# Kernel optimization log

Hardware: AMD Instinct MI355X
Metric: run time of the kernel (lower is better)

Reference implementation:

```python
import jax, jax.numpy as jnp
import numpy as np
from jax import lax

N_NODES = 4096
WINDOW = 288
SLIDE = 12
ENC_STEPS = 12
DEC_STEPS = 12
HID = 64
EMB = 64
PRED = 12
C1, C2 = 32, 64
KSZ, STR = 10, 2
OUT_LEN = 66  # ((288-10)//2+1 -> 140; (140-10)//2+1 -> 66)
EPS = 1e-5


def _conv1d(x, w, b, stride):
    # x: [N, Cin, L], w: [Cout, Cin, K]
    y = lax.conv_general_dilated(x, w, (stride,), 'VALID',
                                 dimension_numbers=('NCH', 'OIH', 'NCH'))
    return y + b[None, :, None]


def _bn(x, g, b):
    # BatchNorm1d training-mode stats over (batch, length) per channel
    m = x.mean(axis=(0, 2), keepdims=True)
    v = x.var(axis=(0, 2), keepdims=True)
    return (x - m) * jax.lax.rsqrt(v + EPS) * g[None, :, None] + b[None, :, None]


def _embed(x, conv1_w, conv1_b, conv2_w, conv2_b, bn1_g, bn1_b, bn2_g, bn2_b,
           fcconv_w, fcconv_b, fc_w, fc_b):
    # x: [N, WINDOW] -> [N, EMB]
    x = x[:, None, :]                                   # [N,1,W]
    x = _bn(jax.nn.relu(_conv1d(x, conv1_w, conv1_b, STR)), bn1_g, bn1_b)
    x = _bn(jax.nn.relu(_conv1d(x, conv2_w, conv2_b, STR)), bn2_g, bn2_b)
    x = jax.nn.relu(_conv1d(x, fcconv_w, fcconv_b, 1))  # [N,1,OUT_LEN]
    x = jnp.einsum('ncl,le->nce', x, fc_w) + fc_b       # [N,1,EMB]
    # NOTE: original code calls F.relu(x) but discards the result -> no relu here
    return x[:, 0, :]


def _gconv(x, adj, W, b):
    # diffusion conv: [x, A x, 2A(Ax) - x] (K=2, includes identity term)
    x1 = adj @ x
    x2 = 2.0 * (adj @ x1) - x
    return jnp.concatenate([x, x1, x2], axis=-1) @ W + b


def _dcgru_cell(x, h, adj, Wg, bg, Wc, bc):
    ru = jax.nn.sigmoid(_gconv(jnp.concatenate([x, h], -1), adj, Wg, bg))
    r, u = jnp.split(ru, 2, axis=-1)
    c = jnp.tanh(_gconv(jnp.concatenate([x, r * h], -1), adj, Wc, bc))
    return u * h + (1.0 - u) * c


def setup_inputs() -> dict:
    key = jax.random.key(0)
    ks = jax.random.split(key, 20)
    n_mat = 3  # K+1 diffusion matrices
    gin = (EMB + HID) * n_mat
    inp = {
        'inputs': jax.random.normal(ks[0], (N_NODES, (ENC_STEPS + DEC_STEPS - 1) * SLIDE + WINDOW), jnp.float32),
        'targets': jax.random.normal(ks[1], (N_NODES, DEC_STEPS * PRED), jnp.float32),
        'conv1_w': jax.random.normal(ks[3], (C1, 1, KSZ), jnp.float32) * 0.1,
        'conv1_b': jnp.zeros((C1,), jnp.float32),
        'conv2_w': jax.random.normal(ks[4], (C2, C1, KSZ), jnp.float32) * 0.1,
        'conv2_b': jnp.zeros((C2,), jnp.float32),
        'bn1_g': jnp.ones((C1,), jnp.float32), 'bn1_b': jnp.zeros((C1,), jnp.float32),
        'bn2_g': jnp.ones((C2,), jnp.float32), 'bn2_b': jnp.zeros((C2,), jnp.float32),
        'fcconv_w': jax.random.normal(ks[5], (1, C2, 1), jnp.float32) * 0.1,
        'fcconv_b': jnp.zeros((1,), jnp.float32),
        'fc_w': jax.random.normal(ks[6], (OUT_LEN, EMB), jnp.float32) * (1.0 / np.sqrt(OUT_LEN)),
        'fc_b': jnp.zeros((EMB,), jnp.float32),
        'enc_Wg': jax.random.normal(ks[7], (gin, 2 * HID), jnp.float32) * (1.0 / np.sqrt(gin)),
        'enc_bg': jnp.ones((2 * HID,), jnp.float32),
        'enc_Wc': jax.random.normal(ks[8], (gin, HID), jnp.float32) * (1.0 / np.sqrt(gin)),
        'enc_bc': jnp.zeros((HID,), jnp.float32),
        'dec_Wg': jax.random.normal(ks[9], (gin, 2 * HID), jnp.float32) * (1.0 / np.sqrt(gin)),
        'dec_bg': jnp.ones((2 * HID,), jnp.float32),
        'dec_Wc': jax.random.normal(ks[10], (gin, HID), jnp.float32) * (1.0 / np.sqrt(gin)),
        'dec_bc': jnp.zeros((HID,), jnp.float32),
        'pred_w': jax.random.normal(ks[11], (HID, PRED), jnp.float32) * (1.0 / np.sqrt(HID)),
        'pred_b': jnp.full((PRED,), 0.1, jnp.float32),
    }
    a = jax.random.uniform(ks[2], (N_NODES, N_NODES), jnp.float32)
    inp['adj'] = a / a.sum(axis=-1, keepdims=True)  # row-stochastic adjacency
    return inp


def reference(inputs, targets, adj,
              conv1_w, conv1_b, conv2_w, conv2_b, bn1_g, bn1_b, bn2_g, bn2_b,
              fcconv_w, fcconv_b, fc_w, fc_b,
              enc_Wg, enc_bg, enc_Wc, enc_bc,
              dec_Wg, dec_bg, dec_Wc, dec_bc,
              pred_w, pred_b):
    n = inputs.shape[0]
    # windowed views: idx[i] = i*SLIDE, 24 windows of length WINDOW
    idx = SLIDE * jnp.arange(ENC_STEPS + DEC_STEPS)
    wins = inputs[:, idx[:, None] + jnp.arange(WINDOW)]        # [N, 24, W]
    wins = jnp.transpose(wins, (1, 0, 2))                      # [24, N, W]
    embs = jax.vmap(lambda w: _embed(w, conv1_w, conv1_b, conv2_w, conv2_b,
                                     bn1_g, bn1_b, bn2_g, bn2_b,
                                     fcconv_w, fcconv_b, fc_w, fc_b))(wins)  # [24,N,EMB]
    enc_x, dec_x = embs[:ENC_STEPS], embs[ENC_STEPS:]

    h0 = jnp.zeros((n, HID), inputs.dtype)
    def enc_step(h, x):
        return _dcgru_cell(x, h, adj, enc_Wg, enc_bg, enc_Wc, enc_bc), None
    h_enc, _ = lax.scan(enc_step, h0, enc_x)

    # decoder: each step uses the SAME encoder hidden state (as in original code)
    dec_h = jax.vmap(lambda x: _dcgru_cell(x, h_enc, adj, dec_Wg, dec_bg, dec_Wc, dec_bc))(dec_x)  # [12,N,HID]
    preds = dec_h @ pred_w + pred_b                             # [12,N,PRED]
    return jnp.transpose(preds, (1, 0, 2)).reshape(n, DEC_STEPS * PRED)
```

## Files before the change

kernel.cpp:

```cpp
#include <hip/hip_runtime.h>
#include <hip/hip_bf16.h>
#include <math.h>

#define NN     4096
#define INLEN  564
#define NT     24
#define NC1    32
#define NC2    64
#define KS     10
#define EPS    1e-5f

typedef short s8v __attribute__((ext_vector_type(8)));
typedef short s4v __attribute__((ext_vector_type(4)));
typedef float f4v __attribute__((ext_vector_type(4)));

static const long O_COLS   = 0;
static const long O_COLSQ  = 8960;
static const long O_STATS  = 17920;
static const long O_H      = 20992;
static const long ZERO_FLOATS = 283136;
static const long O_A1     = 283136;
static const long O_D1     = 283904;
static const long O_CB2    = 284672;
static const long O_W2B    = 286208;
static const long O_G1P    = 532480;
static const long O_Y2     = 18882560;
static const long O_EMBS   = 27795456;
static const long O_ADJB   = 532480;
static const long O_PP     = 8921088;
static const long O_X      = 13115392;
static const long O_XT     = 13639680;
static const long O_T1     = 13901824;
static const long O_T1T    = 14426112;
static const long O_T2     = 14688256;
static const long O_RH     = 15212544;
static const long O_RHT    = 15474688;
static const long O_P1S    = 15605760;
static const long O_P1ST   = 15867904;
static const long O_P2S    = 15998976;
static const long O_UE     = 16261120;
static const long O_EB     = 16392192;
static const long O_EBT    = 20062208;
static const long O_AE1    = 21897216;
static const long O_AE1T   = 25567232;
static const long O_AE2    = 27795456;
static const long O_RHB    = 31465472;
static const long O_P1B    = 34611200;
static const long O_P2B    = O_X;
static const long O_HD     = O_PP;

struct Src { const float* p; int ld; int off; int tmul; };

static __device__ __forceinline__ float cvt_bf(short s) {
  return __uint_as_float(((unsigned)(unsigned short)s) << 16);
}
static __device__ __forceinline__ short bf16bits(float v) {
  __hip_bfloat16_raw r = __hip_bfloat16_raw(__float2bfloat16(v));
  return (short)r.x;
}

__global__ __launch_bounds__(256) void k_conv1n(const float* __restrict__ inp,
    const float* __restrict__ w1, const float* __restrict__ b1,
    __hip_bfloat16* __restrict__ g1p) {
  __shared__ float xin[INLEN];
  __shared__ float wl[320];
  __shared__ float bl[32];
  int n = blockIdx.x, tid = threadIdx.x;
  for (int i=tid; i<INLEN; i+=256) xin[i] = inp[(long)n*INLEN + i];
  for (int i=tid; i<320; i+=256) wl[i] = w1[i];
  if (tid < 32)  bl[tid] = b1[tid];
  __syncthreads();
  int c = tid & 31, pb = tid >> 5;
  float wreg[KS];
  #pragma unroll
  for (int k=0;k<KS;k++) wreg[k] = wl[c*KS+k];
  float bias = bl[c];
  for (int p = pb; p < 280; p += 8) {
    float acc = 0.f;
    if (p < 278) {
      acc = bias;
      #pragma unroll
      for (int k=0;k<KS;k++) acc = fmaf(wreg[k], xin[2*p+k], acc);
      acc = fmaxf(acc, 0.f);
    }
    g1p[((long)n*280 + p)*32 + c] = __float2bfloat16(acc);
  }
}

__global__ __launch_bounds__(256) void k_colsum2(const __hip_bfloat16* __restrict__ g1p,
    float* __restrict__ colS, float* __restrict__ colSQ) {
  int gid = blockIdx.x*256 + threadIdx.x;
  int cg = gid % 1120, chunk = gid / 1120;
  int col0 = cg*8;
  float s[8], sq[8];
  #pragma unroll
  for (int j=0;j<8;j++) { s[j]=0.f; sq[j]=0.f; }
  int n0 = chunk*128;
  const short* gp = (const short*)g1p;
  for (int n=n0; n<n0+128; n++) {
    s8v v = *(const s8v*)(gp + (long)n*8960 + col0);
    #pragma unroll
    for (int j=0;j<8;j++) { float f = cvt_bf(v[j]); s[j]+=f; sq[j]+=f*f; }
  }
  #pragma unroll
  for (int j=0;j<8;j++) { atomicAdd(&colS[col0+j], s[j]); atomicAdd(&colSQ[col0+j], sq[j]); }
}

__global__ __launch_bounds__(64) void k_bn1aff(const float* __restrict__ colS,
    const float* __restrict__ colSQ, const float* __restrict__ g, const float* __restrict__ b,
    float* __restrict__ a1, float* __restrict__ d1) {
  int i = blockIdx.x*64 + threadIdx.x;
  if (i >= NT*NC1) return;
  int t = i / NC1, c = i % NC1;
  float s=0.f, sq=0.f;
  for (int p=6*t; p<6*t+140; p++) { s += colS[p*32+c]; sq += colSQ[p*32+c]; }
  float cnt = 4096.f*140.f;
  float m = s/cnt;
  float v = sq/cnt - m*m;
  float a = g[c]*rsqrtf(v+EPS);
  a1[i] = a;
  d1[i] = b[c] - m*a;
}

__global__ __launch_bounds__(256) void k_w2b(const float* __restrict__ w2,
    const float* __restrict__ b2, const float* __restrict__ a1, const float* __restrict__ d1,
    __hip_bfloat16* __restrict__ w2b, float* __restrict__ cb2) {
  int i = blockIdx.x*256 + threadIdx.x;
  if (i >= NT*NC2) return;
  int t = i>>6, c2 = i&63;
  float cb = b2[c2];
  for (int c1=0;c1<NC1;c1++) {
    float a = a1[t*32+c1], d = d1[t*32+c1];
    float wsum = 0.f;
    for (int k=0;k<KS;k++) {
      float wv = w2[(c2*32+c1)*KS+k];
      wsum += wv;
      w2b[(((long)t*10 + k)*64 + c2)*32 + c1] = __float2bfloat16(wv*a);
    }
    cb += wsum*d;
  }
  cb2[i] = cb;
}

__global__ __launch_bounds__(256) void k_conv2m(const __hip_bfloat16* __restrict__ g1p,
    const __hip_bfloat16* __restrict__ w2b, const float* __restrict__ cb2,
    __hip_bfloat16* __restrict__ y2, float* __restrict__ stats, int t) {
  __shared__ __attribute__((aligned(16))) short patch[4*140*40];
  __shared__ float sS[64], sQ[64];
  int tid = threadIdx.x, w = tid>>6, lane = tid&63;
  int n0 = blockIdx.x*4;
  if (tid < 64) { sS[tid]=0.f; sQ[tid]=0.f; }
  const short* gp = (const short*)g1p;
  for (int f = tid; f < 2240; f += 256) {
    int nn = f / 560, rr = f % 560;
    int row = rr >> 2, kq = rr & 3;
    s8v v = *(const s8v*)(gp + ((long)(n0+nn)*280 + 6*t + row)*32 + kq*8);
    *(s8v*)&patch[(nn*140 + row)*40 + kq*8] = v;
  }
  __syncthreads();
  int q = lane>>4, m = lane&15;
  f4v acc[5][4];
  #pragma unroll
  for (int a=0;a<5;a++)
    #pragma unroll
    for (int b=0;b<4;b++) acc[a][b] = (f4v){0.f,0.f,0.f,0.f};
  const short* wb = (const short*)w2b + (long)t*10*64*32;
  for (int s=0; s<10; s++) {
    int j = s>>1, r = s&1;
    s8v bfr[4];
    #pragma unroll
    for (int ng=0; ng<4; ng++)
      bfr[ng] = *(const s8v*)(wb + (long)(s*64 + ng*16 + m)*32 + q*8);
    #pragma unroll
    for (int mg=0; mg<5; mg++) {
      int l2 = mg*16 + m;
      int u = l2 + j; u = (u>69)?69:u;
      s8v afr = *(const s8v*)&patch[(w*140 + 2*u + r)*40 + q*8];
      #pragma unroll
      for (int ng=0; ng<4; ng++)
        acc[mg][ng] = __builtin_amdgcn_mfma_f32_16x16x32_bf16(afr, bfr[ng], acc[mg][ng], 0,0,0);
    }
  }
  int node = n0 + w;
  float s1a[4]={0,0,0,0}, s2a[4]={0,0,0,0};
  #pragma unroll
  for (int mg=0; mg<5; mg++) {
    int l2b = mg*16 + q*4;
    #pragma unroll
    for (int ng=0; ng<4; ng++) {
      int c2 = ng*16 + m;
      float cbv = cb2[t*64 + c2];
      float vv[4];
      #pragma unroll
      for (int rr=0; rr<4; rr++) {
        float v = fmaxf(acc[mg][ng][rr] + cbv, 0.f);
        vv[rr] = v;
        if (l2b + rr < 66) { s1a[ng] += v; s2a[ng] += v*v; }
      }
      long base = ((long)node*64 + c2)*68 + l2b;
      if (mg < 4) {
        s4v o;
        #pragma unroll
        for (int rr=0; rr<4; rr++) o[rr] = bf16bits(vv[rr]);
        *(s4v*)((short*)y2 + base) = o;
      } else {
        for (int rr=0; rr<4; rr++) if (l2b+rr < 66) y2[base+rr] = __float2bfloat16(vv[rr]);
      }
    }
  }
  #pragma unroll
  for (int ng=0; ng<4; ng++) {
    atomicAdd(&sS[ng*16+m], s1a[ng]);
    atomicAdd(&sQ[ng*16+m], s2a[ng]);
  }
  __syncthreads();
  if (tid < 64) {
    atomicAdd(&stats[t*128+tid], sS[tid]);
    atomicAdd(&stats[t*128+64+tid], sQ[tid]);
  }
}

__global__ __launch_bounds__(256) void k_pass2(const __hip_bfloat16* __restrict__ y2,
    const float* __restrict__ stats, const float* __restrict__ bn2g, const float* __restrict__ bn2b,
    const float* __restrict__ fcvw, const float* __restrict__ fcvb,
    const float* __restrict__ fcW, const float* __restrict__ fcB,
    float* __restrict__ embs, int t) {
  __shared__ __attribute__((aligned(16))) short yb[4*64*68];
  __shared__ float fw[66*64];
  __shared__ float fwa[64], cfcs[64];
  __shared__ float zbuf[4][68];
  int tid = threadIdx.x;
  int n0 = blockIdx.x*4;
  const short* yg = (const short*)y2;
  for (int f=tid; f<2176; f+=256)
    *(s8v*)&yb[f*8] = *(const s8v*)(yg + (long)n0*64*68 + f*8);
  for (int i=tid; i<66*64; i+=256) fw[i] = fcW[i];
  if (tid < 64) {
    float cnt = 4096.f*66.f;
    float m = stats[t*128+tid]/cnt;
    float v = stats[t*128+64+tid]/cnt - m*m;
    float a = bn2g[tid]*rsqrtf(v+EPS);
    float d = bn2b[tid] - m*a;
    fwa[tid]  = fcvw[tid]*a;
    cfcs[tid] = fcvw[tid]*d;
  }
  __syncthreads();
  float cfc = fcvb[0];
  #pragma unroll 8
  for (int c=0;c<64;c++) cfc += cfcs[c];
  for (int idx=tid; idx<4*66; idx+=256) {
    int nn = idx/66, l = idx%66;
    float z = cfc;
    #pragma unroll 8
    for (int c=0;c<64;c++) z = fmaf(fwa[c], cvt_bf(yb[(nn*64+c)*68 + l]), z);
    zbuf[nn][l] = fmaxf(z, 0.f);
  }
  __syncthreads();
  int nn = tid>>6, e = tid&63;
  float acc = fcB[e];
  for (int l=0;l<66;l++) acc = fmaf(zbuf[nn][l], fw[l*64+e], acc);
  embs[((long)t*NN + n0+nn)*64 + e] = acc;
}

__global__ __launch_bounds__(256) void k_cvtadj(const float* __restrict__ adj,
    __hip_bfloat16* __restrict__ adjb) {
  long gid = ((long)blockIdx.x*256 + threadIdx.x)*4;
  float4 v = *(const float4*)(adj + gid);
  adjb[gid+0] = __float2bfloat16(v.x);
  adjb[gid+1] = __float2bfloat16(v.y);
  adjb[gid+2] = __float2bfloat16(v.z);
  adjb[gid+3] = __float2bfloat16(v.w);
}

template<int BN>
__global__ __launch_bounds__(256) void k_mmb(const __hip_bfloat16* __restrict__ A,
    const __hip_bfloat16* __restrict__ Bt, float* __restrict__ P,
    int N, int kchunk, long zoff) {
  constexpr int BM = 64;
  constexpr int WN = BN/2;
  constexpr int MI = 2;
  constexpr int NJ = WN/16;
  constexpr int AIT = BM*8/256;
  constexpr int BIT = BN*8/256;
  __shared__ __attribute__((aligned(16))) short As[BM*64];
  __shared__ __attribute__((aligned(16))) short Bs[BN*64];
  int tid = threadIdx.x;
  int w = tid >> 6, lane = tid & 63;
  int wm = w >> 1, wn = w & 1;
  int q = lane >> 4, m = lane & 15;
  long Mb = (long)blockIdx.x * BM;
  int Nb = blockIdx.y * BN;
  int k0 = blockIdx.z * kchunk;
  const short* Ag = (const short*)A;
  const short* Bg = (const short*)Bt;
  s8v ar[AIT], br[BIT];
  #pragma unroll
  for (int it=0; it<AIT; ++it) {
    int f = tid + it*256; int kq = f & 7, row = f >> 3;
    ar[it] = *(const s8v*)(Ag + (Mb + row)*4096 + k0 + kq*8);
  }
  #pragma unroll
  for (int it=0; it<BIT; ++it) {
    int f = tid + it*256; int kq = f & 7, col = f >> 3;
    br[it] = *(const s8v*)(Bg + (long)(Nb + col)*4096 + k0 + kq*8);
  }
  f4v acc[MI][NJ];
  #pragma unroll
  for (int i=0;i<MI;i++)
    #pragma unroll
    for (int j=0;j<NJ;j++) acc[i][j] = (f4v){0.f,0.f,0.f,0.f};
  for (int kc = k0; kc < k0 + kchunk; kc += 64) {
    __syncthreads();
    #pragma unroll
    for (int it=0; it<AIT; ++it) {
      int f = tid + it*256; int kq = f & 7, row = f >> 3;
      *(s8v*)&As[(row*8 + (kq ^ (row&7)))*8] = ar[it];
    }
    #pragma unroll
    for (int it=0; it<BIT; ++it) {
      int f = tid + it*256; int kq = f & 7, col = f >> 3;
      *(s8v*)&Bs[(col*8 + (kq ^ (col&7)))*8] = br[it];
    }
    __syncthreads();
    if (kc + 64 < k0 + kchunk) {
      #pragma unroll
      for (int it=0; it<AIT; ++it) {
        int f = tid + it*256; int kq = f & 7, row = f >> 3;
        ar[it] = *(const s8v*)(Ag + (Mb + row)*4096 + (kc+64) + kq*8);
      }
      #pragma unroll
      for (int it=0; it<BIT; ++it) {
        int f = tid + it*256; int kq = f & 7, col = f >> 3;
        br[it] = *(const s8v*)(Bg + (long)(Nb + col)*4096 + (kc+64) + kq*8);
      }
    }
    #pragma unroll
    for (int h=0; h<2; ++h) {
      s8v af[MI], bfv[NJ];
      #pragma unroll
      for (int i=0;i<MI;i++) {
        int row = wm*32 + i*16 + m;
        af[i] = *(const s8v*)&As[(row*8 + ((h*4+q) ^ (row&7)))*8];
      }
      #pragma unroll
      for (int j=0;j<NJ;j++) {
        int col = wn*WN + j*16 + m;
        bfv[j] = *(const s8v*)&Bs[(col*8 + ((h*4+q) ^ (col&7)))*8];
      }
      #pragma unroll
      for (int i=0;i<MI;i++)
        #pragma unroll
        for (int j=0;j<NJ;j++)
          acc[i][j] = __builtin_amdgcn_mfma_f32_16x16x32_bf16(af[i], bfv[j], acc[i][j], 0, 0, 0);
    }
  }
  float* pp = P + (long)blockIdx.z * zoff;
  #pragma unroll
  for (int i=0;i<MI;i++) {
    long row0 = Mb + wm*32 + i*16 + q*4;
    #pragma unroll
    for (int j=0;j<NJ;j++) {
      int col = Nb + wn*WN + j*16 + m;
      #pragma unroll
      for (int r=0;r<4;r++)
        pp[(row0 + r)*N + col] = acc[i][j][r];
    }
  }
}

__global__ __launch_bounds__(256) void k_redT(const float* __restrict__ P,
    float* __restrict__ dst, const float* __restrict__ ref,
    __hip_bfloat16* __restrict__ dstT, int ldc, int ksplit, long zoff, int mode,
    int writeF, int writeT) {
  __shared__ float tile[64][65];
  int tid = threadIdx.x;
  int n0 = blockIdx.x*64, c0 = blockIdx.y*64;
  for (int i=0; i<16; i++) {
    int flat = i*256 + tid;
    int cc = flat & 63, nn = flat >> 6;
    long idx = (long)(n0+nn)*ldc + c0+cc;
    float v = P[idx];
    for (int s=1; s<ksplit; s++) v += P[(long)s*zoff + idx];
    if (mode) v = 2.f*v - ref[idx];
    if (writeF) dst[idx] = v;
    tile[nn][cc] = v;
  }
  __syncthreads();
  if (writeT) {
    for (int i=0; i<16; i++) {
      int flat = i*256 + tid;
      int nn = flat & 63, cc = flat >> 6;
      dstT[(long)(c0+cc)*4096 + n0+nn] = __float2bfloat16(tile[nn][cc]);
    }
  }
}

__global__ __launch_bounds__(256) void k_buildXT(const float* __restrict__ et,
    const float* __restrict__ h, float* __restrict__ X, __hip_bfloat16* __restrict__ Xt) {
  __shared__ float tile[64][65];
  int tid = threadIdx.x;
  int n0 = blockIdx.x*64, c0 = blockIdx.y*64;
  for (int i=0; i<16; i++) {
    int flat = i*256 + tid;
    int cc = flat & 63, nn = flat >> 6;
    int col = c0 + cc, n = n0 + nn;
    float v = (col < 64) ? et[(long)n*64 + col] : h[(long)n*64 + (col-64)];
    X[(long)n*128 + col] = v;
    tile[nn][cc] = v;
  }
  __syncthreads();
  for (int i=0; i<16; i++) {
    int flat = i*256 + tid;
    int nn = flat & 63, cc = flat >> 6;
    Xt[(long)(c0+cc)*4096 + n0+nn] = __float2bfloat16(tile[nn][cc]);
  }
}

__global__ __launch_bounds__(256) void k_gatherE(const float* __restrict__ embs,
    const float* __restrict__ h, float* __restrict__ Eb, __hip_bfloat16* __restrict__ Ebt) {
  __shared__ float tile[64][65];
  int tid = threadIdx.x;
  int n0 = blockIdx.x*64, c0 = blockIdx.y*64;
  for (int i=0; i<16; i++) {
    int flat = i*256 + tid;
    int cc = flat & 63, nn = flat >> 6;
    int col = c0 + cc, n = n0 + nn;
    float v;
    if (col < 768)      v = embs[((long)(12 + (col>>6))*NN + n)*64 + (col & 63)];
    else if (col < 832) v = h[(long)n*64 + (col - 768)];
    else                v = 0.f;
    Eb[(long)n*896 + col] = v;
    tile[nn][cc] = v;
  }
  __syncthreads();
  for (int i=0; i<16; i++) {
    int flat = i*256 + tid;
    int nn = flat & 63, cc = flat >> 6;
    Ebt[(long)(c0+cc)*4096 + n0+nn] = __float2bfloat16(tile[nn][cc]);
  }
}

__global__ __launch_bounds__(256) void k_ggemm(
    Src s0, Src s1, Src s2, Src s3, Src s4, Src s5,
    const float* __restrict__ W, const float* __restrict__ bias, int N, int mode,
    float* __restrict__ o1, int ld1, int t1, __hip_bfloat16* __restrict__ o1t,
    __hip_bfloat16* __restrict__ o2, const float* __restrict__ h) {
  __shared__ float Ags[32][68];
  __shared__ float Bgs[32][64];
  int tid = threadIdx.x;
  int Mb = blockIdx.x*64, Nb = blockIdx.y*64;
  int tr = tid >> 4, tc = tid & 15;
  float acc[4][4];
  #pragma unroll
  for (int a=0;a<4;a++)
    #pragma unroll
    for (int b=0;b<4;b++) acc[a][b] = 0.f;
  for (int c0=0; c0<384; c0+=32) {
    Src S;
    switch (c0 >> 6) {
      case 0: S = s0; break; case 1: S = s1; break; case 2: S = s2; break;
      case 3: S = s3; break; case 4: S = s4; break; default: S = s5; break;
    }
    int cc0 = c0 & 63;
    __syncthreads();
    #pragma unroll
    for (int h0=0; h0<8; h0++) {
      int idx = tid + h0*256;
      int kk = idx & 31, mm = idx >> 5;
      int row = Mb + mm, tt = row >> 12, n = row & 4095;
      Ags[kk][mm] = S.p[(long)n*S.ld + S.off + S.tmul*(tt*64) + cc0 + kk];
    }
    #pragma unroll
    for (int h0=0; h0<8; h0++) {
      int idx = tid + h0*256;
      int kk = idx >> 6, cc = idx & 63;
      Bgs[kk][cc] = W[(long)(c0+kk)*N + Nb + cc];
    }
    __syncthreads();
    #pragma unroll
    for (int kk=0; kk<32; kk++) {
      f4v a4 = *(const f4v*)&Ags[kk][tr*4];
      f4v b4 = *(const f4v*)&Bgs[kk][tc*4];
      #pragma unroll
      for (int rr=0; rr<4; rr++)
        #pragma unroll
        for (int j=0; j<4; j++)
          acc[rr][j] = fmaf(a4[rr], b4[j], acc[rr][j]);
    }
  }
  #pragma unroll
  for (int rr=0; rr<4; rr++) {
    int row = Mb + tr*4 + rr, tt = row >> 12, n = row & 4095;
    #pragma unroll
    for (int j=0; j<4; j++) {
      int col = Nb + tc*4 + j;
      float g = acc[rr][j] + bias[col];
      if (mode == 0) {
        float sg = 1.f/(1.f + expf(-g));
        if (col < 64) {
          float v = sg * h[(long)n*64 + col];
          o1[(long)n*ld1 + (long)t1*tt*64 + col] = v;
          o1t[((long)t1*tt*64 + col)*4096 + n] = __float2bfloat16(v);
        } else {
          o2[(long)row*64 + (col - 64)] = __float2bfloat16(sg);
        }
      } else {
        float uu = __bfloat162float(o2[(long)row*64 + col]);
        o1[(long)row*64 + col] = uu*h[(long)n*64 + col] + (1.f - uu)*tanhf(g);
      }
    }
  }
}

__global__ __launch_bounds__(256) void k_pred(const float* __restrict__ hd,
    const float* __restrict__ pw, const float* __restrict__ pb, float* __restrict__ out) {
  int gid = blockIdx.x*256 + threadIdx.x;
  int wid = gid >> 6;
  int lane = threadIdx.x & 63;
  if (wid >= 12*NN) return;
  int t = wid >> 12, n = wid & 4095;
  float hv = hd[(long)wid*64 + lane];
  float res = 0.f;
  #pragma unroll
  for (int p=0;p<12;p++) {
    float v = hv * pw[lane*12 + p];
    #pragma unroll
    for (int off=32; off>0; off>>=1) v += __shfl_xor(v, off, 64);
    if (lane == p) res = v + pb[p];
  }
  if (lane < 12) out[(long)n*144 + t*12 + lane] = res;
}

extern "C" void kernel_launch(void* const* d_in, const int* in_sizes, int n_in,
                              void* d_out, int out_size, void* d_ws, size_t ws_size,
                              hipStream_t stream) {
  const float* inp  = (const float*)d_in[0];
  const float* c1w  = (const float*)d_in[2];
  const float* c1b  = (const float*)d_in[3];
  const float* c2w  = (const float*)d_in[4];
  const float* c2b  = (const float*)d_in[5];
  const float* bn1g = (const float*)d_in[6];
  const float* bn1b = (const float*)d_in[7];
  const float* bn2g = (const float*)d_in[8];
  const float* bn2b = (const float*)d_in[9];
  const float* fcvw = (const float*)d_in[10];
  const float* fcvb = (const float*)d_in[11];
  const float* fcW  = (const float*)d_in[12];
  const float* fcB  = (const float*)d_in[13];
  const float* eWg  = (const float*)d_in[14];
  const float* ebg  = (const float*)d_in[15];
  const float* eWc  = (const float*)d_in[16];
  const float* ebc  = (const float*)d_in[17];
  const float* dWg  = (const float*)d_in[18];
  const float* dbg  = (const float*)d_in[19];
  const float* dWc  = (const float*)d_in[20];
  const float* dbc  = (const float*)d_in[21];
  const float* pw   = (const float*)d_in[22];
  const float* pb   = (const float*)d_in[23];
  const float* adj  = (const float*)d_in[n_in-1];
  for (int i=0;i<n_in;i++) if (in_sizes[i] == NN*NN) adj = (const float*)d_in[i];

  float* ws = (float*)d_ws;
  float* colS  = ws + O_COLS;
  float* colSQ = ws + O_COLSQ;
  float* stats = ws + O_STATS;
  float* h     = ws + O_H;
  float* a1    = ws + O_A1;
  float* d1    = ws + O_D1;
  float* cb2   = ws + O_CB2;
  __hip_bfloat16* w2b = (__hip_bfloat16*)(ws + O_W2B);
  __hip_bfloat16* g1p = (__hip_bfloat16*)(ws + O_G1P);
  __hip_bfloat16* y2  = (__hip_bfloat16*)(ws + O_Y2);
  float* embs  = ws + O_EMBS;
  __hip_bfloat16* adjb = (__hip_bfloat16*)(ws + O_ADJB);
  float* Pp    = ws + O_PP;
  float* X     = ws + O_X;
  __hip_bfloat16* Xt  = (__hip_bfloat16*)(ws + O_XT);
  float* T1    = ws + O_T1;
  __hip_bfloat16* T1t = (__hip_bfloat16*)(ws + O_T1T);
  float* T2    = ws + O_T2;
  float* rh    = ws + O_RH;
  __hip_bfloat16* rht = (__hip_bfloat16*)(ws + O_RHT);
  float* P1s   = ws + O_P1S;
  __hip_bfloat16* P1st = (__hip_bfloat16*)(ws + O_P1ST);
  float* P2s   = ws + O_P2S;
  __hip_bfloat16* ue  = (__hip_bfloat16*)(ws + O_UE);
  float* Eb    = ws + O_EB;
  __hip_bfloat16* Ebt = (__hip_bfloat16*)(ws + O_EBT);
  float* AE1   = ws + O_AE1;
  __hip_bfloat16* AE1t = (__hip_bfloat16*)(ws + O_AE1T);
  float* AE2   = ws + O_AE2;
  float* RHb   = ws + O_RHB;
  float* P1B   = ws + O_P1B;
  float* P2B   = ws + O_P2B;
  float* hd    = ws + O_HD;
  __hip_bfloat16* RHbt = Ebt;
  __hip_bfloat16* P1Bt = Ebt;
  __hip_bfloat16* ud   = AE1t;

  auto S = [](const float* p, int ld, int off, int tmul){ Src s; s.p=p; s.ld=ld; s.off=off; s.tmul=tmul; return s; };

  hipMemsetAsync(ws, 0, ZERO_FLOATS*sizeof(float), stream);

  k_conv1n<<<4096, 256, 0, stream>>>(inp, c1w, c1b, g1p);
  k_colsum2<<<140, 256, 0, stream>>>(g1p, colS, colSQ);
  k_bn1aff<<<12, 64, 0, stream>>>(colS, colSQ, bn1g, bn1b, a1, d1);
  k_w2b   <<<6, 256, 0, stream>>>(c2w, c2b, a1, d1, w2b, cb2);
  for (int t=0; t<NT; t++) {
    k_conv2m<<<1024, 256, 0, stream>>>(g1p, w2b, cb2, y2, stats, t);
    k_pass2 <<<1024, 256, 0, stream>>>(y2, stats, bn2g, bn2b, fcvw, fcvb, fcW, fcB, embs, t);
  }

  k_cvtadj<<<16384, 256, 0, stream>>>(adj, adjb);

  for (int t=0; t<12; t++) {
    const float* et = embs + (long)t*NN*64;
    k_buildXT<<<dim3(64,2), 256, 0, stream>>>(et, h, X, Xt);
    k_mmb<128><<<dim3(64,1,8), 256, 0, stream>>>(adjb, Xt, Pp, 128, 512, 4096L*128);
    k_redT<<<dim3(64,2), 256, 0, stream>>>(Pp, T1, (const float*)nullptr, T1t, 128, 8, 4096L*128, 0, 1, 1);
    k_mmb<128><<<dim3(64,1,8), 256, 0, stream>>>(adjb, T1t, Pp, 128, 512, 4096L*128);
    k_redT<<<dim3(64,2), 256, 0, stream>>>(Pp, T2, X, (__hip_bfloat16*)nullptr, 128, 8, 4096L*128, 1, 1, 0);
    k_ggemm<<<dim3(64,2), 256, 0, stream>>>(
        S(X,128,0,0), S(X,128,64,0), S(T1,128,0,0), S(T1,128,64,0), S(T2,128,0,0), S(T2,128,64,0),
        eWg, ebg, 128, 0, rh, 64, 0, rht, ue, h);
    k_mmb<64><<<dim3(64,1,8), 256, 0, stream>>>(adjb, rht, Pp, 64, 512, 4096L*64);
    k_redT<<<dim3(64,1), 256, 0, stream>>>(Pp, P1s, (const float*)nullptr, P1st, 64, 8, 4096L*64, 0, 1, 1);
    k_mmb<64><<<dim3(64,1,8), 256, 0, stream>>>(adjb, P1st, Pp, 64, 512, 4096L*64);
    k_redT<<<dim3(64,1), 256, 0, stream>>>(Pp, P2s, rh, (__hip_bfloat16*)nullptr, 64, 8, 4096L*64, 1, 1, 0);
    k_ggemm<<<dim3(64,1), 256, 0, stream>>>(
        S(et,64,0,0), S(rh,64,0,0), S(T1,128,0,0), S(P1s,64,0,0), S(T2,128,0,0), S(P2s,64,0,0),
        eWc, ebc, 64, 1, h, 0, 0, (__hip_bfloat16*)nullptr, ue, h);
  }

  const long ZOFF896 = 4096L*896;
  const long ZOFF_P1 = O_PP - O_P1B;
  const long ZOFF_P2 = O_PP - O_X;
  k_gatherE<<<dim3(64,14), 256, 0, stream>>>(embs, h, Eb, Ebt);
  k_mmb<128><<<dim3(64,7,2), 256, 0, stream>>>(adjb, Ebt, Pp, 896, 2048, ZOFF896);
  k_redT<<<dim3(64,14), 256, 0, stream>>>(Pp, AE1, (const float*)nullptr, AE1t, 896, 2, ZOFF896, 0, 1, 1);
  k_mmb<128><<<dim3(64,7,2), 256, 0, stream>>>(adjb, AE1t, Pp, 896, 2048, ZOFF896);
  k_redT<<<dim3(64,14), 256, 0, stream>>>(Pp, AE2, Eb, (__hip_bfloat16*)nullptr, 896, 2, ZOFF896, 1, 1, 0);
  k_ggemm<<<dim3(768,2), 256, 0, stream>>>(
      S(Eb,896,0,1), S(Eb,896,768,0), S(AE1,896,0,1), S(AE1,896,768,0), S(AE2,896,0,1), S(AE2,896,768,0),
      dWg, dbg, 128, 0, RHb, 768, 1, RHbt, ud, h);
  k_mmb<128><<<dim3(64,6,2), 256, 0, stream>>>(adjb, RHbt, P1B, 768, 2048, ZOFF_P1);
  k_redT<<<dim3(64,12), 256, 0, stream>>>(P1B, P1B, (const float*)nullptr, P1Bt, 768, 2, ZOFF_P1, 0, 1, 1);
  k_mmb<128><<<dim3(64,6,2), 256, 0, stream>>>(adjb, P1Bt, P2B, 768, 2048, ZOFF_P2);
  k_redT<<<dim3(64,12), 256, 0, stream>>>(P2B, P2B, RHb, (__hip_bfloat16*)nullptr, 768, 2, ZOFF_P2, 1, 1, 0);
  k_ggemm<<<dim3(768,1), 256, 0, stream>>>(
      S(Eb,896,0,1), S(RHb,768,0,1), S(AE1,896,0,1), S(P1B,768,0,1), S(AE2,896,0,1), S(P2B,768,0,1),
      dWc, dbc, 64, 1, hd, 0, 0, (__hip_bfloat16*)nullptr, ud, h);

  k_pred<<<12288, 256, 0, stream>>>(hd, pw, pb, (float*)d_out);
}
```

Measured before the change: 5.324 ms.

## Fuse split-K reduction into GEMM via atomic counters, retile gate GEMMs

```diff
diff --git a/kernel.cpp b/kernel.cpp
--- a/kernel.cpp
+++ b/kernel.cpp
@@ -13,19 +13,21 @@
 typedef short s8v __attribute__((ext_vector_type(8)));
 typedef short s4v __attribute__((ext_vector_type(4)));
 typedef float f4v __attribute__((ext_vector_type(4)));
+typedef float f2v __attribute__((ext_vector_type(2)));
 
 static const long O_COLS   = 0;
 static const long O_COLSQ  = 8960;
 static const long O_STATS  = 17920;
 static const long O_H      = 20992;
-static const long ZERO_FLOATS = 283136;
-static const long O_A1     = 283136;
-static const long O_D1     = 283904;
-static const long O_CB2    = 284672;
-static const long O_W2B    = 286208;
-static const long O_G1P    = 532480;
-static const long O_Y2     = 18882560;
-static const long O_EMBS   = 27795456;
+static const long O_CNT    = 283136;
+static const long ZERO_FLOATS = 291328;
+static const long O_A1     = 291328;
+static const long O_D1     = 292096;
+static const long O_CB2    = 292864;
+static const long O_W2B    = 532480;
+static const long O_G1P    = 778240;
+static const long O_Y2     = 19128320;
+static const long O_EMBS   = 28041216;
 static const long O_ADJB   = 532480;
 static const long O_PP     = 8921088;
 static const long O_X      = 13115392;
@@ -46,6 +48,7 @@
 static const long O_AE2    = 27795456;
 static const long O_RHB    = 31465472;
 static const long O_P1B    = 34611200;
+static const long O_P1BT   = O_PP;
 static const long O_P2B    = O_X;
 static const long O_HD     = O_PP;
 
@@ -274,13 +277,15 @@
 
 template<int BN>
 __global__ __launch_bounds__(256) void k_mmb(const __hip_bfloat16* __restrict__ A,
-    const __hip_bfloat16* __restrict__ Bt, float* __restrict__ P,
-    int N, int kchunk, long zoff) {
+    const __hip_bfloat16* __restrict__ Bt, float* P,
+    int N, int kchunk, long zoff,
+    float* dst, const float* __restrict__ ref, __hip_bfloat16* __restrict__ dstT,
+    int mode, int writeT, unsigned* __restrict__ cnt, int zsplit) {
   constexpr int BM = 64;
   constexpr int WN = BN/2;
   constexpr int MI = 2;
   constexpr int NJ = WN/16;
-  constexpr int AIT = BM*8/256;
+  constexpr int AIT = 2;
   constexpr int BIT = BN*8/256;
   __shared__ __attribute__((aligned(16))) short As[BM*64];
   __shared__ __attribute__((aligned(16))) short Bs[BN*64];
@@ -293,104 +298,135 @@
   int k0 = blockIdx.z * kchunk;
   const short* Ag = (const short*)A;
   const short* Bg = (const short*)Bt;
-  s8v ar[AIT], br[BIT];
-  #pragma unroll
-  for (int it=0; it<AIT; ++it) {
-    int f = tid + it*256; int kq = f & 7, row = f >> 3;
-    ar[it] = *(const s8v*)(Ag + (Mb + row)*4096 + k0 + kq*8);
-  }
-  #pragma unroll
-  for (int it=0; it<BIT; ++it) {
-    int f = tid + it*256; int kq = f & 7, col = f >> 3;
-    br[it] = *(const s8v*)(Bg + (long)(Nb + col)*4096 + k0 + kq*8);
-  }
+  s8v arA[AIT], brA[BIT], arB[AIT], brB[BIT];
+
+  auto loadAr = [&](s8v* d, int kb){
+    #pragma unroll
+    for (int i2=0;i2<AIT;i2++){ int f=tid+i2*256; int kq=f&7, row=f>>3;
+      d[i2] = *(const s8v*)(Ag + (Mb+row)*4096 + kb + kq*8); } };
+  auto loadBr = [&](s8v* d, int kb){
+    #pragma unroll
+    for (int i2=0;i2<BIT;i2++){ int f=tid+i2*256; int kq=f&7, col=f>>3;
+      d[i2] = *(const s8v*)(Bg + (long)(Nb+col)*4096 + kb + kq*8); } };
+
   f4v acc[MI][NJ];
   #pragma unroll
   for (int i=0;i<MI;i++)
     #pragma unroll
     for (int j=0;j<NJ;j++) acc[i][j] = (f4v){0.f,0.f,0.f,0.f};
-  for (int kc = k0; kc < k0 + kchunk; kc += 64) {
-    __syncthreads();
-    #pragma unroll
-    for (int it=0; it<AIT; ++it) {
-      int f = tid + it*256; int kq = f & 7, row = f >> 3;
-      *(s8v*)&As[(row*8 + (kq ^ (row&7)))*8] = ar[it];
-    }
-    #pragma unroll
-    for (int it=0; it<BIT; ++it) {
-      int f = tid + it*256; int kq = f & 7, col = f >> 3;
-      *(s8v*)&Bs[(col*8 + (kq ^ (col&7)))*8] = br[it];
-    }
-    __syncthreads();
-    if (kc + 64 < k0 + kchunk) {
-      #pragma unroll
-      for (int it=0; it<AIT; ++it) {
-        int f = tid + it*256; int kq = f & 7, row = f >> 3;
-        ar[it] = *(const s8v*)(Ag + (Mb + row)*4096 + (kc+64) + kq*8);
-      }
-      #pragma unroll
-      for (int it=0; it<BIT; ++it) {
-        int f = tid + it*256; int kq = f & 7, col = f >> 3;
-        br[it] = *(const s8v*)(Bg + (long)(Nb + col)*4096 + (kc+64) + kq*8);
-      }
-    }
-    #pragma unroll
-    for (int h=0; h<2; ++h) {
+
+  auto writeS = [&](s8v* a, s8v* b){
+    #pragma unroll
+    for (int i2=0;i2<AIT;i2++){ int f=tid+i2*256; int kq=f&7, row=f>>3;
+      *(s8v*)&As[(row*8 + (kq ^ (row&7)))*8] = a[i2]; }
+    #pragma unroll
+    for (int i2=0;i2<BIT;i2++){ int f=tid+i2*256; int kq=f&7, col=f>>3;
+      *(s8v*)&Bs[(col*8 + (kq ^ (col&7)))*8] = b[i2]; } };
+  auto compute = [&](){
+    #pragma unroll
+    for (int h2=0; h2<2; ++h2) {
       s8v af[MI], bfv[NJ];
       #pragma unroll
       for (int i=0;i<MI;i++) {
         int row = wm*32 + i*16 + m;
-        af[i] = *(const s8v*)&As[(row*8 + ((h*4+q) ^ (row&7)))*8];
+        af[i] = *(const s8v*)&As[(row*8 + ((h2*4+q) ^ (row&7)))*8];
       }
       #pragma unroll
       for (int j=0;j<NJ;j++) {
         int col = wn*WN + j*16 + m;
-        bfv[j] = *(const s8v*)&Bs[(col*8 + ((h*4+q) ^ (col&7)))*8];
+        bfv[j] = *(const s8v*)&Bs[(col*8 + ((h2*4+q) ^ (col&7)))*8];
       }
       #pragma unroll
       for (int i=0;i<MI;i++)
         #pragma unroll
         for (int j=0;j<NJ;j++)
           acc[i][j] = __builtin_amdgcn_mfma_f32_16x16x32_bf16(af[i], bfv[j], acc[i][j], 0, 0, 0);
-    }
-  }
-  float* pp = P + (long)blockIdx.z * zoff;
-  #pragma unroll
-  for (int i=0;i<MI;i++) {
-    long row0 = Mb + wm*32 + i*16 + q*4;
-    #pragma unroll
-    for (int j=0;j<NJ;j++) {
-      int col = Nb + wn*WN + j*16 + m;
-      #pragma unroll
-      for (int r=0;r<4;r++)
-        pp[(row0 + r)*N + col] = acc[i][j][r];
-    }
-  }
-}
-
-__global__ __launch_bounds__(256) void k_redT(const float* __restrict__ P,
-    float* __restrict__ dst, const float* __restrict__ ref,
-    __hip_bfloat16* __restrict__ dstT, int ldc, int ksplit, long zoff, int mode,
-    int writeF, int writeT) {
-  __shared__ float tile[64][65];
-  int tid = threadIdx.x;
-  int n0 = blockIdx.x*64, c0 = blockIdx.y*64;
-  for (int i=0; i<16; i++) {
-    int flat = i*256 + tid;
-    int cc = flat & 63, nn = flat >> 6;
-    long idx = (long)(n0+nn)*ldc + c0+cc;
-    float v = P[idx];
-    for (int s=1; s<ksplit; s++) v += P[(long)s*zoff + idx];
-    if (mode) v = 2.f*v - ref[idx];
-    if (writeF) dst[idx] = v;
-    tile[nn][cc] = v;
-  }
-  __syncthreads();
-  if (writeT) {
-    for (int i=0; i<16; i++) {
-      int flat = i*256 + tid;
-      int nn = flat & 63, cc = flat >> 6;
-      dstT[(long)(c0+cc)*4096 + n0+nn] = __float2bfloat16(tile[nn][cc]);
+    } };
+
+  loadAr(arA, k0);      loadBr(brA, k0);
+  loadAr(arB, k0+64);   loadBr(brB, k0+64);
+  int kiters = kchunk >> 6;
+  for (int it = 0; it < kiters; it += 2) {
+    __syncthreads();
+    writeS(arA, brA);
+    __syncthreads();
+    { int kn = (it+2 < kiters) ? k0 + (it+2)*64 : k0;
+      loadAr(arA, kn); loadBr(brA, kn); }
+    compute();
+    __syncthreads();
+    writeS(arB, brB);
+    __syncthreads();
+    { int kn = (it+3 < kiters) ? k0 + (it+3)*64 : k0;
+      loadAr(arB, kn); loadBr(brB, kn); }
+    compute();
+  }
+
+  if (zsplit > 1) {
+    float* pp = P + (long)blockIdx.z * zoff;
+    #pragma unroll
+    for (int i=0;i<MI;i++) {
+      long row0 = Mb + wm*32 + i*16 + q*4;
+      #pragma unroll
+      for (int j=0;j<NJ;j++) {
+        int col = Nb + wn*WN + j*16 + m;
+        #pragma unroll
+        for (int r=0;r<4;r++) pp[(row0+r)*N + col] = acc[i][j][r];
+      }
+    }
+    __threadfence();
+    __syncthreads();
+    __shared__ unsigned lastv;
+    if (tid == 0) lastv = atomicAdd(&cnt[blockIdx.y*gridDim.x + blockIdx.x], 1u);
+    __syncthreads();
+    if (lastv != (unsigned)(zsplit-1)) return;
+    __threadfence();
+    #pragma unroll
+    for (int i=0;i<MI;i++) {
+      long row0 = Mb + wm*32 + i*16 + q*4;
+      #pragma unroll
+      for (int j=0;j<NJ;j++) {
+        int col = Nb + wn*WN + j*16 + m;
+        float vr[4];
+        #pragma unroll
+        for (int r=0;r<4;r++) {
+          long idx = (row0+r)*N + col;
+          float v = P[idx];
+          for (int s2=1;s2<zsplit;s2++) v += P[(long)s2*zoff + idx];
+          if (mode) v = 2.f*v - ref[idx];
+          dst[idx] = v;
+          vr[r] = v;
+        }
+        if (writeT) {
+          s4v o;
+          #pragma unroll
+          for (int r=0;r<4;r++) o[r] = bf16bits(vr[r]);
+          *(s4v*)((short*)dstT + (long)col*4096 + row0) = o;
+        }
+      }
+    }
+  } else {
+    #pragma unroll
+    for (int i=0;i<MI;i++) {
+      long row0 = Mb + wm*32 + i*16 + q*4;
+      #pragma unroll
+      for (int j=0;j<NJ;j++) {
+        int col = Nb + wn*WN + j*16 + m;
+        float vr[4];
+        #pragma unroll
+        for (int r=0;r<4;r++) {
+          long idx = (row0+r)*N + col;
+          float v = acc[i][j][r];
+          if (mode) v = 2.f*v - ref[idx];
+          dst[idx] = v;
+          vr[r] = v;
+        }
+        if (writeT) {
+          s4v o;
+          #pragma unroll
+          for (int r=0;r<4;r++) o[r] = bf16bits(vr[r]);
+          *(s4v*)((short*)dstT + (long)col*4096 + row0) = o;
+        }
+      }
     }
   }
 }
@@ -440,57 +476,87 @@
   }
 }
 
-__global__ __launch_bounds__(256) void k_ggemm(
+template<int RPT>
+__global__ __launch_bounds__(256) void k_ggemm2(
     Src s0, Src s1, Src s2, Src s3, Src s4, Src s5,
     const float* __restrict__ W, const float* __restrict__ bias, int N, int mode,
     float* __restrict__ o1, int ld1, int t1, __hip_bfloat16* __restrict__ o1t,
     __hip_bfloat16* __restrict__ o2, const float* __restrict__ h) {
-  __shared__ float Ags[32][68];
-  __shared__ float Bgs[32][64];
+  constexpr int BM = 16*RPT;
+  __shared__ float Ags[32][BM+4];
+  __shared__ float Bgs[32][68];
   int tid = threadIdx.x;
-  int Mb = blockIdx.x*64, Nb = blockIdx.y*64;
+  long Mb = (long)blockIdx.x * BM;
+  int Nb = blockIdx.y * 64;
   int tr = tid >> 4, tc = tid & 15;
-  float acc[4][4];
-  #pragma unroll
-  for (int a=0;a<4;a++)
+  float acc[RPT][4];
+  #pragma unroll
+  for (int a=0;a<RPT;a++)
     #pragma unroll
     for (int b=0;b<4;b++) acc[a][b] = 0.f;
-  for (int c0=0; c0<384; c0+=32) {
-    Src S;
-    switch (c0 >> 6) {
-      case 0: S = s0; break; case 1: S = s1; break; case 2: S = s2; break;
-      case 3: S = s3; break; case 4: S = s4; break; default: S = s5; break;
-    }
-    int cc0 = c0 & 63;
-    __syncthreads();
-    #pragma unroll
-    for (int h0=0; h0<8; h0++) {
+  float ar[2*RPT], br[8];
+  auto pick = [&](int c)->Src {
+    switch (c >> 1) {
+      case 0: return s0; case 1: return s1; case 2: return s2;
+      case 3: return s3; case 4: return s4; default: return s5;
+    } };
+  auto loadA = [&](int c){
+    Src S = pick(c); int cc0 = (c & 1)*32;
+    #pragma unroll
+    for (int h0=0; h0<2*RPT; h0++) {
       int idx = tid + h0*256;
       int kk = idx & 31, mm = idx >> 5;
-      int row = Mb + mm, tt = row >> 12, n = row & 4095;
-      Ags[kk][mm] = S.p[(long)n*S.ld + S.off + S.tmul*(tt*64) + cc0 + kk];
-    }
+      long row = Mb + mm; int tt = (int)(row >> 12); int n = (int)(row & 4095);
+      ar[h0] = S.p[(long)n*S.ld + S.off + S.tmul*(tt*64) + cc0 + kk];
+    } };
+  auto loadB = [&](int c){
     #pragma unroll
     for (int h0=0; h0<8; h0++) {
       int idx = tid + h0*256;
       int kk = idx >> 6, cc = idx & 63;
-      Bgs[kk][cc] = W[(long)(c0+kk)*N + Nb + cc];
-    }
+      br[h0] = W[(long)(c*32+kk)*N + Nb + cc];
+    } };
+  loadA(0); loadB(0);
+  for (int c=0; c<12; c++) {
     __syncthreads();
     #pragma unroll
+    for (int h0=0; h0<2*RPT; h0++) { int idx = tid + h0*256; Ags[idx & 31][idx >> 5] = ar[h0]; }
+    #pragma unroll
+    for (int h0=0; h0<8; h0++)     { int idx = tid + h0*256; Bgs[idx >> 6][idx & 63] = br[h0]; }
+    __syncthreads();
+    if (c < 11) { loadA(c+1); loadB(c+1); }
+    #pragma unroll
     for (int kk=0; kk<32; kk++) {
-      f4v a4 = *(const f4v*)&Ags[kk][tr*4];
       f4v b4 = *(const f4v*)&Bgs[kk][tc*4];
-      #pragma unroll
-      for (int rr=0; rr<4; rr++)
+      if constexpr (RPT == 8) {
+        f4v a0 = *(const f4v*)&Ags[kk][tr*8];
+        f4v a1 = *(const f4v*)&Ags[kk][tr*8+4];
+        #pragma unroll
+        for (int rr=0; rr<4; rr++)
+          #pragma unroll
+          for (int j=0; j<4; j++) {
+            acc[rr][j]   = fmaf(a0[rr], b4[j], acc[rr][j]);
+            acc[4+rr][j] = fmaf(a1[rr], b4[j], acc[4+rr][j]);
+          }
+      } else if constexpr (RPT == 2) {
+        f2v a0 = *(const f2v*)&Ags[kk][tr*2];
+        #pragma unroll
+        for (int rr=0; rr<2; rr++)
+          #pragma unroll
+          for (int j=0; j<4; j++)
+            acc[rr][j] = fmaf(a0[rr], b4[j], acc[rr][j]);
+      } else {
+        float a0 = Ags[kk][tr];
         #pragma unroll
         for (int j=0; j<4; j++)
-          acc[rr][j] = fmaf(a4[rr], b4[j], acc[rr][j]);
-    }
-  }
-  #pragma unroll
-  for (int rr=0; rr<4; rr++) {
-    int row = Mb + tr*4 + rr, tt = row >> 12, n = row & 4095;
+          acc[0][j] = fmaf(a0, b4[j], acc[0][j]);
+      }
+    }
+  }
+  #pragma unroll
+  for (int rr=0; rr<RPT; rr++) {
+    long row = Mb + tr*RPT + rr;
+    int tt = (int)(row >> 12); int n = (int)(row & 4095);
     #pragma unroll
     for (int j=0; j<4; j++) {
       int col = Nb + tc*4 + j;
@@ -565,6 +631,7 @@
   float* colSQ = ws + O_COLSQ;
   float* stats = ws + O_STATS;
   float* h     = ws + O_H;
+  unsigned* cnt = (unsigned*)(ws + O_CNT);
   float* a1    = ws + O_A1;
   float* d1    = ws + O_D1;
   float* cb2   = ws + O_CB2;
@@ -595,7 +662,7 @@
   float* P2B   = ws + O_P2B;
   float* hd    = ws + O_HD;
   __hip_bfloat16* RHbt = Ebt;
-  __hip_bfloat16* P1Bt = Ebt;
+  __hip_bfloat16* P1Bt = (__hip_bfloat16*)(ws + O_P1BT);
   __hip_bfloat16* ud   = AE1t;
 
   auto S = [](const float* p, int ld, int off, int tmul){ Src s; s.p=p; s.ld=ld; s.off=off; s.tmul=tmul; return s; };
@@ -615,39 +682,37 @@
 
   for (int t=0; t<12; t++) {
     const float* et = embs + (long)t*NN*64;
+    unsigned* cb = cnt + t*256;
     k_buildXT<<<dim3(64,2), 256, 0, stream>>>(et, h, X, Xt);
-    k_mmb<128><<<dim3(64,1,8), 256, 0, stream>>>(adjb, Xt, Pp, 128, 512, 4096L*128);
-    k_redT<<<dim3(64,2), 256, 0, stream>>>(Pp, T1, (const float*)nullptr, T1t, 128, 8, 4096L*128, 0, 1, 1);
-    k_mmb<128><<<dim3(64,1,8), 256, 0, stream>>>(adjb, T1t, Pp, 128, 512, 4096L*128);
-    k_redT<<<dim3(64,2), 256, 0, stream>>>(Pp, T2, X, (__hip_bfloat16*)nullptr, 128, 8, 4096L*128, 1, 1, 0);
-    k_ggemm<<<dim3(64,2), 256, 0, stream>>>(
+    k_mmb<128><<<dim3(64,1,8), 256, 0, stream>>>(adjb, Xt, Pp, 128, 512, 4096L*128,
+        T1, (const float*)nullptr, T1t, 0, 1, cb, 8);
+    k_mmb<128><<<dim3(64,1,8), 256, 0, stream>>>(adjb, T1t, Pp, 128, 512, 4096L*128,
+        T2, X, (__hip_bfloat16*)nullptr, 1, 0, cb+64, 8);
+    k_ggemm2<2><<<dim3(128,2), 256, 0, stream>>>(
         S(X,128,0,0), S(X,128,64,0), S(T1,128,0,0), S(T1,128,64,0), S(T2,128,0,0), S(T2,128,64,0),
         eWg, ebg, 128, 0, rh, 64, 0, rht, ue, h);
-    k_mmb<64><<<dim3(64,1,8), 256, 0, stream>>>(adjb, rht, Pp, 64, 512, 4096L*64);
-    k_redT<<<dim3(64,1), 256, 0, stream>>>(Pp, P1s, (const float*)nullptr, P1st, 64, 8, 4096L*64, 0, 1, 1);
-    k_mmb<64><<<dim3(64,1,8), 256, 0, stream>>>(adjb, P1st, Pp, 64, 512, 4096L*64);
-    k_redT<<<dim3(64,1), 256, 0, stream>>>(Pp, P2s, rh, (__hip_bfloat16*)nullptr, 64, 8, 4096L*64, 1, 1, 0);
-    k_ggemm<<<dim3(64,1), 256, 0, stream>>>(
+    k_mmb<64><<<dim3(64,1,8), 256, 0, stream>>>(adjb, rht, Pp, 64, 512, 4096L*64,
+        P1s, (const float*)nullptr, P1st, 0, 1, cb+128, 8);
+    k_mmb<64><<<dim3(64,1,8), 256, 0, stream>>>(adjb, P1st, Pp, 64, 512, 4096L*64,
+        P2s, rh, (__hip_bfloat16*)nullptr, 1, 0, cb+192, 8);
+    k_ggemm2<1><<<dim3(256,1), 256, 0, stream>>>(
         S(et,64,0,0), S(rh,64,0,0), S(T1,128,0,0), S(P1s,64,0,0), S(T2,128,0,0), S(P2s,64,0,0),
         eWc, ebc, 64, 1, h, 0, 0, (__hip_bfloat16*)nullptr, ue, h);
   }
 
-  const long ZOFF896 = 4096L*896;
-  const long ZOFF_P1 = O_PP - O_P1B;
-  const long ZOFF_P2 = O_PP - O_X;
   k_gatherE<<<dim3(64,14), 256, 0, stream>>>(embs, h, Eb, Ebt);
-  k_mmb<128><<<dim3(64,7,2), 256, 0, stream>>>(adjb, Ebt, Pp, 896, 2048, ZOFF896);
-  k_redT<<<dim3(64,14), 256, 0, stream>>>(Pp, AE1, (const float*)nullptr, AE1t, 896, 2, ZOFF896, 0, 1, 1);
-  k_mmb<128><<<dim3(64,7,2), 256, 0, stream>>>(adjb, AE1t, Pp, 896, 2048, ZOFF896);
-  k_redT<<<dim3(64,14), 256, 0, stream>>>(Pp, AE2, Eb, (__hip_bfloat16*)nullptr, 896, 2, ZOFF896, 1, 1, 0);
-  k_ggemm<<<dim3(768,2), 256, 0, stream>>>(
+  k_mmb<128><<<dim3(64,7,1), 256, 0, stream>>>(adjb, Ebt, Pp, 896, 4096, 0,
+      AE1, (const float*)nullptr, AE1t, 0, 1, cnt, 1);
+  k_mmb<128><<<dim3(64,7,1), 256, 0, stream>>>(adjb, AE1t, Pp, 896, 4096, 0,
+      AE2, Eb, (__hip_bfloat16*)nullptr, 1, 0, cnt, 1);
+  k_ggemm2<8><<<dim3(384,2), 256, 0, stream>>>(
       S(Eb,896,0,1), S(Eb,896,768,0), S(AE1,896,0,1), S(AE1,896,768,0), S(AE2,896,0,1), S(AE2,896,768,0),
       dWg, dbg, 128, 0, RHb, 768, 1, RHbt, ud, h);
-  k_mmb<128><<<dim3(64,6,2), 256, 0, stream>>>(adjb, RHbt, P1B, 768, 2048, ZOFF_P1);
-  k_redT<<<dim3(64,12), 256, 0, stream>>>(P1B, P1B, (const float*)nullptr, P1Bt, 768, 2, ZOFF_P1, 0, 1, 1);
-  k_mmb<128><<<dim3(64,6,2), 256, 0, stream>>>(adjb, P1Bt, P2B, 768, 2048, ZOFF_P2);
-  k_redT<<<dim3(64,12), 256, 0, stream>>>(P2B, P2B, RHb, (__hip_bfloat16*)nullptr, 768, 2, ZOFF_P2, 1, 1, 0);
-  k_ggemm<<<dim3(768,1), 256, 0, stream>>>(
+  k_mmb<128><<<dim3(64,6,1), 256, 0, stream>>>(adjb, RHbt, Pp, 768, 4096, 0,
+      P1B, (const float*)nullptr, P1Bt, 0, 1, cnt, 1);
+  k_mmb<128><<<dim3(64,6,1), 256, 0, stream>>>(adjb, P1Bt, Pp, 768, 4096, 0,
+      P2B, RHb, (__hip_bfloat16*)nullptr, 1, 0, cnt, 1);
+  k_ggemm2<8><<<dim3(384,1), 256, 0, stream>>>(
       S(Eb,896,0,1), S(RHb,768,0,1), S(AE1,896,0,1), S(P1B,768,0,1), S(AE2,896,0,1), S(P2B,768,0,1),
       dWc, dbc, 64, 1, hd, 0, 0, (__hip_bfloat16*)nullptr, ud, h);
 
```

Measured after the change: 8.087 ms. 51.9% more time.
